# Kernel tuning notes

Hardware: AMD Instinct MI355X
Metric: run time of the kernel (lower is better)

The kernel has to match this reference:

```python
import jax, jax.numpy as jnp
import numpy as np

BATCH = 4096
INPUT_SIZE = 512
MAX_TERMS = 8
NUM_HEADS = 4
KERNEL_SIZE = 8  # must equal MAX_TERMS for the original module's math to be consistent
LN_EPS = 1e-5


def setup_inputs() -> dict:
    key = jax.random.key(0)
    k = jax.random.split(key, 6)
    x = jax.random.normal(k[0], (BATCH, INPUT_SIZE), dtype=jnp.float32)
    scale_param = jnp.ones((INPUT_SIZE,), dtype=jnp.float32)
    # ParameterList of num_heads tensors -> stacked along leading head dim
    poly_weights = jax.random.normal(k[1], (NUM_HEADS, INPUT_SIZE, MAX_TERMS), dtype=jnp.float32)
    kernels = jax.random.normal(k[2], (NUM_HEADS, INPUT_SIZE, MAX_TERMS, KERNEL_SIZE), dtype=jnp.float32)
    ln_gamma = jnp.ones((INPUT_SIZE * MAX_TERMS * NUM_HEADS,), dtype=jnp.float32)
    ln_beta = jnp.zeros((INPUT_SIZE * MAX_TERMS * NUM_HEADS,), dtype=jnp.float32)
    return {"x": x, "scale_param": scale_param, "poly_weights": poly_weights,
            "kernels": kernels, "ln_gamma": ln_gamma, "ln_beta": ln_beta}


def reference(x, scale_param, poly_weights, kernels, ln_gamma, ln_beta):
    b = x.shape[0]
    m = kernels.shape[2]  # max_terms
    xs = x * scale_param  # [b, i]
    # Chebyshev recurrence T_0..T_{m-1}; small fixed-length Python loop
    Ts = [jnp.ones_like(xs), xs]
    for _ in range(2, m):
        Ts.append(2.0 * xs * Ts[-1] - Ts[-2])
    x_cheb = jnp.stack(Ts, axis=-1)  # [b, i, m]
    # per-feature batched matmul over all heads at once: [b,h,i,k]
    x_head = jnp.einsum('bim,himk->bhik', x_cheb, kernels)
    # poly_weights broadcast (valid since k == m)
    x_head = x_head * poly_weights[None]  # [b,h,i,k]
    x_head = jax.nn.silu(x_head)
    # torch concatenates per-head flats along dim 1 -> (h, i, k) ordering
    flat = x_head.reshape(b, -1)  # [b, h*i*k]
    # LayerNorm (biased variance, eps=1e-5) over full feature dim
    mean = jnp.mean(flat, axis=-1, keepdims=True)
    var = jnp.mean(jnp.square(flat - mean), axis=-1, keepdims=True)
    out = (flat - mean) * jax.lax.rsqrt(var + LN_EPS) * ln_gamma + ln_beta
    return out
```

## Files before the change

kernel.cpp:

```cpp
#include <hip/hip_runtime.h>

#define BATCH 4096
#define ISZ   512
#define MT    8
#define NH    4
#define KS    8
#define NFEAT (NH * ISZ * KS)
#define LN_EPS 1e-5f
#define ROWS  4

typedef float vfloat4 __attribute__((ext_vector_type(4)));

__device__ __forceinline__ void cheb2mono(const float w[8], float4& m0, float4& m1) {
    m0.x = w[0] - w[2] + w[4] - w[6];
    m0.y = w[1] - 3.f*w[3] + 5.f*w[5] - 7.f*w[7];
    m0.z = 2.f*w[2] - 8.f*w[4] + 18.f*w[6];
    m0.w = 4.f*w[3] - 20.f*w[5] + 56.f*w[7];
    m1.x = 8.f*w[4] - 48.f*w[6];
    m1.y = 16.f*w[5] - 112.f*w[7];
    m1.z = 32.f*w[6];
    m1.w = 64.f*w[7];
}

__global__ void prep_w2(const float* __restrict__ kern, const float* __restrict__ poly,
                        float4* __restrict__ W2) {
    const int f = blockIdx.x * 256 + threadIdx.x;
    const int j = f >> 11;
    const int t = (f >> 2) & 511;
    const int c = f & 3;
    const int base = (f >> 3) * 64 + (f & 7);
    const float p = poly[f];
    float w[8];
    #pragma unroll
    for (int m = 0; m < 8; ++m) w[m] = kern[base + m * 8] * p;
    float4 m0, m1;
    cheb2mono(w, m0, m1);
    W2[(j * 8 + 2 * c    ) * 512 + t] = m0;
    W2[(j * 8 + 2 * c + 1) * 512 + t] = m1;
}

__device__ __forceinline__ float fast_silu(float d) {
    return d * __builtin_amdgcn_rcpf(1.f + __expf(-d));
}

__device__ __forceinline__ float horner8(float4 w0, float4 w1, float x) {
    float s = w1.w;
    s = fmaf(s, x, w1.z);
    s = fmaf(s, x, w1.y);
    s = fmaf(s, x, w1.x);
    s = fmaf(s, x, w0.w);
    s = fmaf(s, x, w0.z);
    s = fmaf(s, x, w0.y);
    s = fmaf(s, x, w0.x);
    return s;
}

__device__ __forceinline__ void make_w(const float* kern, const float* poly,
                                       int f, float4& m0, float4& m1) {
    const int base = (f >> 3) * 64 + (f & 7);
    const float p = poly[f];
    float w[8];
    #pragma unroll
    for (int m = 0; m < 8; ++m) w[m] = kern[base + m * 8] * p;
    cheb2mono(w, m0, m1);
}

template <bool USE_W2>
__global__ __launch_bounds__(512, 4)
void cheb_main(const float* __restrict__ x, const float* __restrict__ scale,
               const float4* __restrict__ W2v, const float* __restrict__ kern,
               const float* __restrict__ poly,
               const float* __restrict__ gamma, const float* __restrict__ beta,
               float* __restrict__ out) {
    __shared__ float xs[ROWS][ISZ];
    __shared__ float red[8][2 * ROWS];

    const int t  = threadIdx.x;
    const int r0 = blockIdx.x * ROWS;

    #pragma unroll
    for (int idx = t; idx < ROWS * ISZ; idx += 512) {
        const int r = idx >> 9, i = idx & 511;
        xs[r][i] = x[(r0 + r) * ISZ + i] * scale[i];
    }
    __syncthreads();

    float sum[ROWS], sq[ROWS];
    #pragma unroll
    for (int r = 0; r < ROWS; ++r) { sum[r] = 0.f; sq[r] = 0.f; }

    #pragma unroll 1
    for (int j = 0; j < 8; ++j) {
        const int i = ((j & 1) << 8) + (t >> 1);
        float xv[ROWS];
        #pragma unroll
        for (int r = 0; r < ROWS; ++r) xv[r] = xs[r][i];
        const float4* Wj = W2v + (size_t)j * 8 * 512 + t;
        #pragma unroll
        for (int c = 0; c < 4; ++c) {
            float4 w0, w1;
            if (USE_W2) {
                w0 = Wj[(2 * c) * 512];
                w1 = Wj[(2 * c + 1) * 512];
            } else {
                make_w(kern, poly, j * 2048 + t * 4 + c, w0, w1);
            }
            #pragma unroll
            for (int r = 0; r < ROWS; ++r) {
                const float s = fast_silu(horner8(w0, w1, xv[r]));
                sum[r] += s;
                sq[r]   = fmaf(s, s, sq[r]);
            }
        }
    }

    #pragma unroll
    for (int off = 32; off > 0; off >>= 1) {
        #pragma unroll
        for (int r = 0; r < ROWS; ++r) {
            sum[r] += __shfl_xor(sum[r], off, 64);
            sq[r]  += __shfl_xor(sq[r],  off, 64);
        }
    }
    const int wave = t >> 6;
    if ((t & 63) == 0) {
        #pragma unroll
        for (int r = 0; r < ROWS; ++r) {
            red[wave][r]        = sum[r];
            red[wave][ROWS + r] = sq[r];
        }
    }
    __syncthreads();

    float rs[ROWS], nm[ROWS];
    {
        const float invN = 1.f / (float)NFEAT;
        #pragma unroll
        for (int r = 0; r < ROWS; ++r) {
            float ts = 0.f, tq = 0.f;
            #pragma unroll
            for (int wv = 0; wv < 8; ++wv) { ts += red[wv][r]; tq += red[wv][ROWS + r]; }
            const float mean = ts * invN;
            rs[r] = rsqrtf(fmaxf(tq * invN - mean * mean, 0.f) + LN_EPS);
            nm[r] = -mean * rs[r];
        }
    }

    #pragma unroll 1
    for (int j = 0; j < 8; ++j) {
        const int i  = ((j & 1) << 8) + (t >> 1);
        const int f0 = j * 2048 + t * 4;
        float xv[ROWS];
        #pragma unroll
        for (int r = 0; r < ROWS; ++r) xv[r] = xs[r][i];
        const float4 g  = *(const float4*)(gamma + f0);
        const float4 bb = *(const float4*)(beta  + f0);
        const float4* Wj = W2v + (size_t)j * 8 * 512 + t;
        vfloat4 rv[ROWS];
        #pragma unroll
        for (int c = 0; c < 4; ++c) {
            float4 w0, w1;
            if (USE_W2) {
                w0 = Wj[(2 * c) * 512];
                w1 = Wj[(2 * c + 1) * 512];
            } else {
                make_w(kern, poly, f0 + c, w0, w1);
            }
            const float gc = (c == 0) ? g.x  : (c == 1) ? g.y  : (c == 2) ? g.z  : g.w;
            const float bc = (c == 0) ? bb.x : (c == 1) ? bb.y : (c == 2) ? bb.z : bb.w;
            #pragma unroll
            for (int r = 0; r < ROWS; ++r) {
                const float s = fast_silu(horner8(w0, w1, xv[r]));
                rv[r][c] = fmaf(fmaf(s, rs[r], nm[r]), gc, bc);
            }
        }
        #pragma unroll
        for (int r = 0; r < ROWS; ++r)
            __builtin_nontemporal_store(rv[r],
                (vfloat4*)(out + (size_t)(r0 + r) * NFEAT + f0));
    }
}

extern "C" void kernel_launch(void* const* d_in, const int* in_sizes, int n_in,
                              void* d_out, int out_size, void* d_ws, size_t ws_size,
                              hipStream_t stream) {
    const float* x     = (const float*)d_in[0];
    const float* scale = (const float*)d_in[1];
    const float* poly  = (const float*)d_in[2];
    const float* kern  = (const float*)d_in[3];
    const float* gamma = (const float*)d_in[4];
    const float* beta  = (const float*)d_in[5];
    float* out = (float*)d_out;

    const size_t W2_BYTES = (size_t)NFEAT * 8 * sizeof(float);
    if (ws_size >= W2_BYTES) {
        float4* W2 = (float4*)d_ws;
        prep_w2<<<NFEAT / 256, 256, 0, stream>>>(kern, poly, W2);
        cheb_main<true><<<BATCH / ROWS, 512, 0, stream>>>(x, scale, (const float4*)W2,
                                                          kern, poly, gamma, beta, out);
    } else {
        cheb_main<false><<<BATCH / ROWS, 512, 0, stream>>>(x, scale, nullptr,
                                                           kern, poly, gamma, beta, out);
    }
}
```

Baseline: 311.2 us.

## Cache SiLU results in registers to avoid recomputing in normalization pass

Each thread keeps its 32 per-row SiLU outputs in registers from the statistics pass and reuses them when writing normalized outputs, instead of recomputing the Horner polynomial and SiLU. To fit register budget, rows per block are reduced from 4 to 2 and the loops are fully unrolled. This halves transcendental and FMA work but doubles weight loads per row and raises register pressure, risking spills or lower occupancy.

```diff
diff --git a/kernel.cpp b/kernel.cpp
--- a/kernel.cpp
+++ b/kernel.cpp
@@ -7,7 +7,6 @@
 #define KS    8
 #define NFEAT (NH * ISZ * KS)
 #define LN_EPS 1e-5f
-#define ROWS  4
 
 typedef float vfloat4 __attribute__((ext_vector_type(4)));
 
@@ -72,29 +71,26 @@
                const float* __restrict__ poly,
                const float* __restrict__ gamma, const float* __restrict__ beta,
                float* __restrict__ out) {
-    __shared__ float xs[ROWS][ISZ];
-    __shared__ float red[8][2 * ROWS];
+    __shared__ float xs[2][ISZ];
+    __shared__ float red[8][4];
 
     const int t  = threadIdx.x;
-    const int r0 = blockIdx.x * ROWS;
+    const int r0 = blockIdx.x * 2;
 
-    #pragma unroll
-    for (int idx = t; idx < ROWS * ISZ; idx += 512) {
+    for (int idx = t; idx < 2 * ISZ; idx += 512) {
         const int r = idx >> 9, i = idx & 511;
         xs[r][i] = x[(r0 + r) * ISZ + i] * scale[i];
     }
     __syncthreads();
 
-    float sum[ROWS], sq[ROWS];
+    float st0[32], st1[32];
+    float sum0 = 0.f, sq0 = 0.f, sum1 = 0.f, sq1 = 0.f;
+
     #pragma unroll
-    for (int r = 0; r < ROWS; ++r) { sum[r] = 0.f; sq[r] = 0.f; }
-
-    #pragma unroll 1
     for (int j = 0; j < 8; ++j) {
-        const int i = ((j & 1) << 8) + (t >> 1);
-        float xv[ROWS];
-        #pragma unroll
-        for (int r = 0; r < ROWS; ++r) xv[r] = xs[r][i];
+        const int i  = ((j & 1) << 8) + (t >> 1);
+        const float xa = xs[0][i];
+        const float xb = xs[1][i];
         const float4* Wj = W2v + (size_t)j * 8 * 512 + t;
         #pragma unroll
         for (int c = 0; c < 4; ++c) {
@@ -105,79 +101,60 @@
             } else {
                 make_w(kern, poly, j * 2048 + t * 4 + c, w0, w1);
             }
-            #pragma unroll
-            for (int r = 0; r < ROWS; ++r) {
-                const float s = fast_silu(horner8(w0, w1, xv[r]));
-                sum[r] += s;
-                sq[r]   = fmaf(s, s, sq[r]);
-            }
+            const float s0 = fast_silu(horner8(w0, w1, xa));
+            const float s1 = fast_silu(horner8(w0, w1, xb));
+            st0[j * 4 + c] = s0;
+            st1[j * 4 + c] = s1;
+            sum0 += s0; sq0 = fmaf(s0, s0, sq0);
+            sum1 += s1; sq1 = fmaf(s1, s1, sq1);
         }
     }
 
     #pragma unroll
     for (int off = 32; off > 0; off >>= 1) {
-        #pragma unroll
-        for (int r = 0; r < ROWS; ++r) {
-            sum[r] += __shfl_xor(sum[r], off, 64);
-            sq[r]  += __shfl_xor(sq[r],  off, 64);
-        }
+        sum0 += __shfl_xor(sum0, off, 64);
+        sq0  += __shfl_xor(sq0,  off, 64);
+        sum1 += __shfl_xor(sum1, off, 64);
+        sq1  += __shfl_xor(sq1,  off, 64);
     }
     const int wave = t >> 6;
     if ((t & 63) == 0) {
-        #pragma unroll
-        for (int r = 0; r < ROWS; ++r) {
-            red[wave][r]        = sum[r];
-            red[wave][ROWS + r] = sq[r];
-        }
+        red[wave][0] = sum0; red[wave][1] = sq0;
+        red[wave][2] = sum1; red[wave][3] = sq1;
     }
     __syncthreads();
 
-    float rs[ROWS], nm[ROWS];
-    {
-        const float invN = 1.f / (float)NFEAT;
-        #pragma unroll
-        for (int r = 0; r < ROWS; ++r) {
-            float ts = 0.f, tq = 0.f;
-            #pragma unroll
-            for (int wv = 0; wv < 8; ++wv) { ts += red[wv][r]; tq += red[wv][ROWS + r]; }
-            const float mean = ts * invN;
-            rs[r] = rsqrtf(fmaxf(tq * invN - mean * mean, 0.f) + LN_EPS);
-            nm[r] = -mean * rs[r];
-        }
+    float ts0 = 0.f, tq0 = 0.f, ts1 = 0.f, tq1 = 0.f;
+    #pragma unroll
+    for (int wv = 0; wv < 8; ++wv) {
+        ts0 += red[wv][0]; tq0 += red[wv][1];
+        ts1 += red[wv][2]; tq1 += red[wv][3];
     }
+    const float invN  = 1.f / (float)NFEAT;
+    const float mean0 = ts0 * invN, mean1 = ts1 * invN;
+    const float rs0 = rsqrtf(fmaxf(tq0 * invN - mean0 * mean0, 0.f) + LN_EPS);
+    const float rs1 = rsqrtf(fmaxf(tq1 * invN - mean1 * mean1, 0.f) + LN_EPS);
+    const float nm0 = -mean0 * rs0;
+    const float nm1 = -mean1 * rs1;
 
-    #pragma unroll 1
+    float* o0 = out + (size_t)r0 * NFEAT;
+    float* o1 = o0 + NFEAT;
+    #pragma unroll
     for (int j = 0; j < 8; ++j) {
-        const int i  = ((j & 1) << 8) + (t >> 1);
         const int f0 = j * 2048 + t * 4;
-        float xv[ROWS];
-        #pragma unroll
-        for (int r = 0; r < ROWS; ++r) xv[r] = xs[r][i];
         const float4 g  = *(const float4*)(gamma + f0);
         const float4 bb = *(const float4*)(beta  + f0);
-        const float4* Wj = W2v + (size_t)j * 8 * 512 + t;
-        vfloat4 rv[ROWS];
-        #pragma unroll
-        for (int c = 0; c < 4; ++c) {
-            float4 w0, w1;
-            if (USE_W2) {
-                w0 = Wj[(2 * c) * 512];
-                w1 = Wj[(2 * c + 1) * 512];
-            } else {
-                make_w(kern, poly, f0 + c, w0, w1);
-            }
-            const float gc = (c == 0) ? g.x  : (c == 1) ? g.y  : (c == 2) ? g.z  : g.w;
-            const float bc = (c == 0) ? bb.x : (c == 1) ? bb.y : (c == 2) ? bb.z : bb.w;
-            #pragma unroll
-            for (int r = 0; r < ROWS; ++r) {
-                const float s = fast_silu(horner8(w0, w1, xv[r]));
-                rv[r][c] = fmaf(fmaf(s, rs[r], nm[r]), gc, bc);
-            }
-        }
-        #pragma unroll
-        for (int r = 0; r < ROWS; ++r)
-            __builtin_nontemporal_store(rv[r],
-                (vfloat4*)(out + (size_t)(r0 + r) * NFEAT + f0));
+        vfloat4 r0v, r1v;
+        r0v.x = fmaf(fmaf(st0[j * 4 + 0], rs0, nm0), g.x, bb.x);
+        r0v.y = fmaf(fmaf(st0[j * 4 + 1], rs0, nm0), g.y, bb.y);
+        r0v.z = fmaf(fmaf(st0[j * 4 + 2], rs0, nm0), g.z, bb.z);
+        r0v.w = fmaf(fmaf(st0[j * 4 + 3], rs0, nm0), g.w, bb.w);
+        r1v.x = fmaf(fmaf(st1[j * 4 + 0], rs1, nm1), g.x, bb.x);
+        r1v.y = fmaf(fmaf(st1[j * 4 + 1], rs1, nm1), g.y, bb.y);
+        r1v.z = fmaf(fmaf(st1[j * 4 + 2], rs1, nm1), g.z, bb.z);
+        r1v.w = fmaf(fmaf(st1[j * 4 + 3], rs1, nm1), g.w, bb.w);
+        __builtin_nontemporal_store(r0v, (vfloat4*)(o0 + f0));
+        __builtin_nontemporal_store(r1v, (vfloat4*)(o1 + f0));
     }
 }
 
@@ -196,10 +173,10 @@
     if (ws_size >= W2_BYTES) {
         float4* W2 = (float4*)d_ws;
         prep_w2<<<NFEAT / 256, 256, 0, stream>>>(kern, poly, W2);
-        cheb_main<true><<<BATCH / ROWS, 512, 0, stream>>>(x, scale, (const float4*)W2,
-                                                          kern, poly, gamma, beta, out);
+        cheb_main<true><<<BATCH / 2, 512, 0, stream>>>(x, scale, (const float4*)W2,
+                                                       kern, poly, gamma, beta, out);
     } else {
-        cheb_main<false><<<BATCH / ROWS, 512, 0, stream>>>(x, scale, nullptr,
-                                                           kern, poly, gamma, beta, out);
+        cheb_main<false><<<BATCH / 2, 512, 0, stream>>>(x, scale, nullptr,
+                                                        kern, poly, gamma, beta, out);
     }
 }
```

Result: no change. 316.1 us (+1.6%).
